# Kernel tuning notes

Measured on AMD Instinct MI355X. Metric: run time of the kernel, lower is better.

Reference implementation:

```python
import jax, jax.numpy as jnp
import numpy as np

B, S = 1024, 64          # batch, num clips (att_size)
R = 1024                 # CG_rnn_size
E = 1024                 # CG_input_encoding_size
CD = 1024                # clip_context_dim
ED = 1024                # event_context_dim
H = 512                  # CG_att_hid_size


def setup_inputs() -> dict:
    key = jax.random.key(0)
    ks = jax.random.split(key, 20)
    s = 0.02
    return {
        "xt": jax.random.normal(ks[0], (B, E), jnp.float32),
        "video": jax.random.normal(ks[1], (B, 1024), jnp.float32),
        "event": jax.random.normal(ks[2], (B, ED), jnp.float32),
        "clip": jax.random.normal(ks[3], (B, S, CD), jnp.float32),
        "clip_mask": jax.random.randint(ks[4], (B, S), 0, 2, jnp.int32),
        "state_h": jax.random.normal(ks[5], (2, B, R), jnp.float32),
        "state_c": jax.random.normal(ks[6], (2, B, R), jnp.float32),
        # LSTMCell 0 (input = event ++ xt -> ED+E)
        "W_ih0": jax.random.normal(ks[7], (4 * R, ED + E), jnp.float32) * s,
        "b_ih0": jnp.zeros((4 * R,), jnp.float32),
        "W_hh0": jax.random.normal(ks[8], (4 * R, R), jnp.float32) * s,
        "b_hh0": jnp.zeros((4 * R,), jnp.float32),
        # LSTMCell 1 (input = att ++ xt -> CD+E)
        "W_ih1": jax.random.normal(ks[9], (4 * R, CD + E), jnp.float32) * s,
        "b_ih1": jnp.zeros((4 * R,), jnp.float32),
        "W_hh1": jax.random.normal(ks[10], (4 * R, R), jnp.float32) * s,
        "b_hh1": jnp.zeros((4 * R,), jnp.float32),
        # Attention params
        "W_ctx": jax.random.normal(ks[11], (H, CD), jnp.float32) * s,
        "b_ctx": jnp.zeros((H,), jnp.float32),
        "W_h2a": jax.random.normal(ks[12], (H, R), jnp.float32) * s,
        "b_h2a": jnp.zeros((H,), jnp.float32),
        "W_alpha": jax.random.normal(ks[13], (1, H), jnp.float32) * s,
        "b_alpha": jnp.zeros((1,), jnp.float32),
    }


def _lstm_cell(x, h, c, W_ih, b_ih, W_hh, b_hh):
    gates = x @ W_ih.T + b_ih + h @ W_hh.T + b_hh  # [B, 4R]
    i, f, g, o = jnp.split(gates, 4, axis=-1)
    i, f, o = jax.nn.sigmoid(i), jax.nn.sigmoid(f), jax.nn.sigmoid(o)
    g = jnp.tanh(g)
    c_new = f * c + i * g
    h_new = o * jnp.tanh(c_new)
    return h_new, c_new


def _attention(h, att_feats, att_mask, W_ctx, b_ctx, W_h2a, b_h2a, W_alpha, b_alpha):
    att = att_feats @ W_ctx.T + b_ctx                 # [B, S, H]
    att_h = h @ W_h2a.T + b_h2a                       # [B, H]
    dot = jnp.tanh(att + att_h[:, None, :])           # [B, S, H]
    scores = (dot @ W_alpha.T + b_alpha)[..., 0]      # [B, S]
    weight = jax.nn.softmax(scores, axis=1)
    m = att_mask.astype(weight.dtype)
    weight = weight * m
    weight = weight / jnp.sum(weight, axis=1, keepdims=True)
    return jnp.einsum('bs,bsd->bd', weight, att_feats)  # [B, CD]


def reference(xt, video, event, clip, clip_mask, state_h, state_c,
              W_ih0, b_ih0, W_hh0, b_hh0, W_ih1, b_ih1, W_hh1, b_hh1,
              W_ctx, b_ctx, W_h2a, b_h2a, W_alpha, b_alpha):
    pre_h1 = state_h[1]
    # stream 0: torch.cat((xt, event), 1)
    h0, c0 = _lstm_cell(jnp.concatenate([xt, event], axis=1),
                        state_h[0], state_c[0], W_ih0, b_ih0, W_hh0, b_hh0)
    att = _attention(pre_h1, clip, clip_mask,
                     W_ctx, b_ctx, W_h2a, b_h2a, W_alpha, b_alpha)
    h1, c1 = _lstm_cell(jnp.concatenate([xt, att], axis=1),
                        state_h[1], state_c[1], W_ih1, b_ih1, W_hh1, b_hh1)
    # dropout layers are identity in eval mode
    output = jnp.concatenate([h0, h1], axis=1)        # [B, 2R]
    new_h = jnp.stack([h0, h1])
    new_c = jnp.stack([c0, c1])
    return output, new_h, new_c
```

## Files before the change

kernel.cpp:

```cpp
#include <hip/hip_runtime.h>

typedef short short8 __attribute__((ext_vector_type(8)));
typedef float floatx4 __attribute__((ext_vector_type(4)));
typedef unsigned short u16;

__device__ __forceinline__ u16 cvt_bf(float x) {
  unsigned u = __float_as_uint(x);
  unsigned r = 0x7FFFu + ((u >> 16) & 1u);
  return (u16)((u + r) >> 16);
}

__device__ __forceinline__ void gll16(const u16* g, u16* l) {
  __builtin_amdgcn_global_load_lds(
      (__attribute__((address_space(1))) void*)(void*)const_cast<u16*>(g),
      (__attribute__((address_space(3))) void*)(void*)l, 16, 0, 0);
}

#define NSEG 11
struct ConvArgs {
  const float* src[NSEG];
  u16* dst[NSEG];
  unsigned lw[NSEG];
  unsigned dstride[NSEG];
  unsigned blk0[NSEG + 1];
};
__global__ __launch_bounds__(256)
void convert_seg(ConvArgs a) {
  const unsigned blk = blockIdx.x;
  int s = 0;
#pragma unroll
  for (int i = 1; i < NSEG; ++i) if (blk >= a.blk0[i]) s = i;
  const unsigned e0 = (blk - a.blk0[s]) * 2048u + threadIdx.x * 8u;
  const float* src = a.src[s] + e0;
  const float4 v0 = *(const float4*)src;
  const float4 v1 = *(const float4*)(src + 4);
  const unsigned row = e0 >> a.lw[s];
  const unsigned col = e0 & ((1u << a.lw[s]) - 1u);
  u16* d = a.dst[s] + (size_t)row * a.dstride[s] + col;
  short8 p;
  p[0] = (short)cvt_bf(v0.x); p[1] = (short)cvt_bf(v0.y);
  p[2] = (short)cvt_bf(v0.z); p[3] = (short)cvt_bf(v0.w);
  p[4] = (short)cvt_bf(v1.x); p[5] = (short)cvt_bf(v1.y);
  p[6] = (short)cvt_bf(v1.z); p[7] = (short)cvt_bf(v1.w);
  *(short8*)d = p;
}

__global__ __launch_bounds__(256, 2)
void gemm_g(const u16* __restrict__ A, int sa,
            const u16* __restrict__ B, int sb,
            const float* __restrict__ bias0, const float* __restrict__ bias1,
            float* __restrict__ out, int N, int K)
{
  __shared__ u16 sA[64 * 64];
  __shared__ u16 sB[128 * 64];

  const int tid = threadIdx.x;
  const int lane = tid & 63, w = tid >> 6;
  const int quad = lane >> 4, l15 = lane & 15;
  const int wm = w >> 1, wn = w & 1;
  const int Mbase = blockIdx.y * 64, Nbase = blockIdx.x * 128;

  const int srow = lane >> 3;
  const int sslot = (lane & 7) ^ (srow & 7);

  floatx4 acc[2][4] = {};

  for (int k0 = 0; k0 < K; k0 += 64) {
    __syncthreads();
#pragma unroll
    for (int j = 0; j < 6; ++j) {
      const int c = w + 4 * j;
      if (c < 8) {
        const int row = c * 8 + srow;
        gll16(A + (size_t)(Mbase + row) * sa + k0 + sslot * 8, &sA[c * 512]);
      } else {
        const int cb = c - 8;
        const int row = cb * 8 + srow;
        gll16(B + (size_t)(Nbase + row) * sb + k0 + sslot * 8, &sB[cb * 512]);
      }
    }
    __syncthreads();

    short8 af[2][2], bf[4][2];
#pragma unroll
    for (int ks = 0; ks < 2; ++ks) {
#pragma unroll
      for (int mt = 0; mt < 2; ++mt) {
        const int row = wm * 32 + mt * 16 + l15;
        const int slot = (ks * 4 + quad) ^ (row & 7);
        af[mt][ks] = *(const short8*)&sA[row * 64 + slot * 8];
      }
#pragma unroll
      for (int nt = 0; nt < 4; ++nt) {
        const int row = wn * 64 + nt * 16 + l15;
        const int slot = (ks * 4 + quad) ^ (row & 7);
        bf[nt][ks] = *(const short8*)&sB[row * 64 + slot * 8];
      }
    }
#pragma unroll
    for (int ks = 0; ks < 2; ++ks)
#pragma unroll
      for (int mt = 0; mt < 2; ++mt)
#pragma unroll
        for (int nt = 0; nt < 4; ++nt)
          acc[mt][nt] = __builtin_amdgcn_mfma_f32_16x16x32_bf16(af[mt][ks], bf[nt][ks], acc[mt][nt], 0, 0, 0);
  }

#pragma unroll
  for (int nt = 0; nt < 4; ++nt) {
    const int col = Nbase + wn * 64 + nt * 16 + l15;
    const float bc = (bias0 ? bias0[col] : 0.f) + (bias1 ? bias1[col] : 0.f);
#pragma unroll
    for (int mt = 0; mt < 2; ++mt) {
      const int rb = Mbase + wm * 32 + mt * 16 + quad * 4;
#pragma unroll
      for (int r = 0; r < 4; ++r)
        out[(size_t)(rb + r) * N + col] = acc[mt][nt][r] + bc;
    }
  }
}

__global__ __launch_bounds__(512)
void clip_scores(const float* __restrict__ clip,
                 const u16* __restrict__ Wc,
                 const float* __restrict__ atth,
                 const float* __restrict__ Walpha,
                 const int* __restrict__ mask,
                 float* __restrict__ wout)
{
  __shared__ u16 sA[64 * 40];
  __shared__ u16 sB[512 * 32];
  __shared__ float wsum[8][64];

  const int b = blockIdx.x;
  const int tid = threadIdx.x;
  const int lane = tid & 63, w = tid >> 6;
  const int quad = lane >> 4, l15 = lane & 15;
  const float* Ab = clip + (size_t)b * 65536;

  floatx4 acc[4][4] = {};

  for (int k0 = 0; k0 < 1024; k0 += 32) {
    __syncthreads();
    {
      const int srow = lane >> 2;
      const int sslot = (lane & 3) ^ (srow & 3);
#pragma unroll
      for (int j = 0; j < 4; ++j) {
        const int c = w + 8 * j;
        const int row = c * 16 + srow;
        gll16(Wc + (size_t)row * 1024 + k0 + sslot * 8, &sB[c * 512]);
      }
    }
    if (w < 4) {
      const int srow = lane >> 2;
      const int scol = (lane & 3) * 8;
      const int row = w * 16 + srow;
      const float* src = Ab + (size_t)row * 1024 + k0 + scol;
      const float4 v0 = *(const float4*)src;
      const float4 v1 = *(const float4*)(src + 4);
      short8 p;
      p[0] = (short)cvt_bf(v0.x); p[1] = (short)cvt_bf(v0.y);
      p[2] = (short)cvt_bf(v0.z); p[3] = (short)cvt_bf(v0.w);
      p[4] = (short)cvt_bf(v1.x); p[5] = (short)cvt_bf(v1.y);
      p[6] = (short)cvt_bf(v1.z); p[7] = (short)cvt_bf(v1.w);
      *(short8*)&sA[row * 40 + scol] = p;
    }
    __syncthreads();

    short8 af[4], bfr[4];
#pragma unroll
    for (int mt = 0; mt < 4; ++mt)
      af[mt] = *(const short8*)&sA[(mt * 16 + l15) * 40 + quad * 8];
#pragma unroll
    for (int nt = 0; nt < 4; ++nt) {
      const int row = w * 64 + nt * 16 + l15;
      const int slot = quad ^ (row & 3);
      bfr[nt] = *(const short8*)&sB[row * 32 + slot * 8];
    }
#pragma unroll
    for (int mt = 0; mt < 4; ++mt)
#pragma unroll
      for (int nt = 0; nt < 4; ++nt)
        acc[mt][nt] = __builtin_amdgcn_mfma_f32_16x16x32_bf16(af[mt], bfr[nt], acc[mt][nt], 0, 0, 0);
  }

  float rs[4][4] = {};
#pragma unroll
  for (int nt = 0; nt < 4; ++nt) {
    const int col = w * 64 + nt * 16 + l15;
    const float wa = Walpha[col];
    const float ah = atth[(size_t)b * 512 + col];
#pragma unroll
    for (int mt = 0; mt < 4; ++mt)
#pragma unroll
      for (int r = 0; r < 4; ++r)
        rs[mt][r] += wa * tanhf(acc[mt][nt][r] + ah);
  }
#pragma unroll
  for (int mt = 0; mt < 4; ++mt)
#pragma unroll
    for (int r = 0; r < 4; ++r) {
      float v = rs[mt][r];
      v += __shfl_xor(v, 1); v += __shfl_xor(v, 2);
      v += __shfl_xor(v, 4); v += __shfl_xor(v, 8);
      if (l15 == 0) wsum[w][mt * 16 + quad * 4 + r] = v;
    }
  __syncthreads();
  if (tid < 64) {
    float s = 0.f;
#pragma unroll
    for (int i = 0; i < 8; ++i) s += wsum[i][tid];
    float mx = s;
#pragma unroll
    for (int d = 32; d; d >>= 1) mx = fmaxf(mx, __shfl_xor(mx, d));
    const float e = expf(s - mx) * (float)mask[b * 64 + tid];
    float den = e;
#pragma unroll
    for (int d = 32; d; d >>= 1) den += __shfl_xor(den, d);
    wout[b * 64 + tid] = e / den;
  }
}

__global__ __launch_bounds__(256)
void ctx_att(const float* __restrict__ clip, const float* __restrict__ wbuf,
             u16* __restrict__ A1)
{
  __shared__ float w[64];
  const int b = blockIdx.x, tid = threadIdx.x;
  if (tid < 64) w[tid] = wbuf[b * 64 + tid];
  __syncthreads();
  const int d4 = tid * 4;
  const float* cb = clip + (size_t)b * 65536 + d4;
  float4 a = make_float4(0.f, 0.f, 0.f, 0.f);
#pragma unroll 8
  for (int s = 0; s < 64; ++s) {
    const float wt = w[s];
    const float4 c = *(const float4*)(cb + (size_t)s * 1024);
    a.x += wt * c.x; a.y += wt * c.y; a.z += wt * c.z; a.w += wt * c.w;
  }
  ushort4 p;
  p.x = cvt_bf(a.x); p.y = cvt_bf(a.y); p.z = cvt_bf(a.z); p.w = cvt_bf(a.w);
  *(ushort4*)&A1[(size_t)b * 3072 + 1024 + d4] = p;
}

__device__ __forceinline__ float sigm(float x) { return 1.0f / (1.0f + expf(-x)); }

__global__ __launch_bounds__(256)
void lstm_ew(const float* __restrict__ gates, const float* __restrict__ cprev,
             float* __restrict__ out, int st)
{
  const int idx = blockIdx.x * 256 + threadIdx.x;
  const int b = idx >> 8;
  const int r4 = (idx & 255) * 4;
  const float* g = gates + (size_t)b * 4096 + r4;
  const float4 gi = *(const float4*)g;
  const float4 gf = *(const float4*)(g + 1024);
  const float4 gg = *(const float4*)(g + 2048);
  const float4 go = *(const float4*)(g + 3072);
  const float4 c  = *(const float4*)(cprev + (size_t)b * 1024 + r4);
  float4 cn, hn;
  cn.x = sigm(gf.x) * c.x + sigm(gi.x) * tanhf(gg.x);  hn.x = sigm(go.x) * tanhf(cn.x);
  cn.y = sigm(gf.y) * c.y + sigm(gi.y) * tanhf(gg.y);  hn.y = sigm(go.y) * tanhf(cn.y);
  cn.z = sigm(gf.z) * c.z + sigm(gi.z) * tanhf(gg.z);  hn.z = sigm(go.z) * tanhf(cn.z);
  cn.w = sigm(gf.w) * c.w + sigm(gi.w) * tanhf(gg.w);  hn.w = sigm(go.w) * tanhf(cn.w);
  *(float4*)(out + (size_t)b * 2048 + st * 1024 + r4) = hn;
  *(float4*)(out + 2097152 + (size_t)st * 1048576 + (size_t)b * 1024 + r4) = hn;
  *(float4*)(out + 4194304 + (size_t)st * 1048576 + (size_t)b * 1024 + r4) = cn;
}

extern "C" void kernel_launch(void* const* d_in, const int* in_sizes, int n_in,
                              void* d_out, int out_size, void* d_ws, size_t ws_size,
                              hipStream_t stream) {
  (void)in_sizes; (void)n_in; (void)out_size; (void)ws_size;
  const float* xt      = (const float*)d_in[0];
  const float* event   = (const float*)d_in[2];
  const float* clip    = (const float*)d_in[3];
  const int*   cmask   = (const int*)d_in[4];
  const float* state_h = (const float*)d_in[5];
  const float* state_c = (const float*)d_in[6];
  const float* W_ih0   = (const float*)d_in[7];
  const float* b_ih0   = (const float*)d_in[8];
  const float* W_hh0   = (const float*)d_in[9];
  const float* b_hh0   = (const float*)d_in[10];
  const float* W_ih1   = (const float*)d_in[11];
  const float* b_ih1   = (const float*)d_in[12];
  const float* W_hh1   = (const float*)d_in[13];
  const float* b_hh1   = (const float*)d_in[14];
  const float* W_ctx   = (const float*)d_in[15];
  const float* b_ctx   = (const float*)d_in[16];
  const float* W_h2a   = (const float*)d_in[17];
  const float* b_h2a   = (const float*)d_in[18];
  const float* W_alpha = (const float*)d_in[19];

  char* w8 = (char*)d_ws;
  float* gates = (float*)(w8 + 0);
  float* att_h = (float*)(w8 + 16777216);
  float* wbuf  = (float*)(w8 + 18874368);
  u16* A0 = (u16*)(w8 + 19136512);
  u16* A1 = (u16*)(w8 + 25427968);
  u16* W0 = (u16*)(w8 + 31719424);
  u16* W1 = (u16*)(w8 + 56885248);
  u16* Wc = (u16*)(w8 + 82051072);
  u16* Wh = (u16*)(w8 + 83099648);

  const float* h0p = state_h;
  const float* h1p = state_h + 1048576;
  const float* c0p = state_c;
  const float* c1p = state_c + 1048576;
  float* out = (float*)d_out;

  ConvArgs ca;
  const float* srcs[NSEG] = {W_ctx, W_h2a, W_ih0, W_hh0, W_ih1, W_hh1,
                             xt, event, h0p, xt, h1p};
  u16* dsts[NSEG] = {Wc, Wh, W0, W0 + 2048, W1, W1 + 2048,
                     A0, A0 + 1024, A0 + 2048, A1, A1 + 2048};
  const unsigned lws[NSEG]  = {10, 10, 11, 10, 11, 10, 10, 10, 10, 10, 10};
  const unsigned dstr[NSEG] = {1024, 1024, 3072, 3072, 3072, 3072,
                               3072, 3072, 3072, 3072, 3072};
  const unsigned nblk[NSEG] = {256, 256, 4096, 2048, 4096, 2048,
                               512, 512, 512, 512, 512};
  unsigned acc_b = 0;
  for (int i = 0; i < NSEG; ++i) {
    ca.src[i] = srcs[i]; ca.dst[i] = dsts[i];
    ca.lw[i] = lws[i]; ca.dstride[i] = dstr[i];
    ca.blk0[i] = acc_b; acc_b += nblk[i];
  }
  ca.blk0[NSEG] = acc_b;
  convert_seg<<<acc_b, 256, 0, stream>>>(ca);

  gemm_g<<<dim3(4, 16), 256, 0, stream>>>(A1 + 2048, 3072, Wh, 1024,
                                          b_h2a, b_ctx, att_h, 512, 1024);

  clip_scores<<<1024, 512, 0, stream>>>(clip, Wc, att_h, W_alpha, cmask, wbuf);

  ctx_att<<<1024, 256, 0, stream>>>(clip, wbuf, A1);

  gemm_g<<<dim3(32, 16), 256, 0, stream>>>(A0, 3072, W0, 3072,
                                           b_ih0, b_hh0, gates, 4096, 3072);
  lstm_ew<<<1024, 256, 0, stream>>>(gates, c0p, out, 0);

  gemm_g<<<dim3(32, 16), 256, 0, stream>>>(A1, 3072, W1, 3072,
                                           b_ih1, b_hh1, gates, 4096, 3072);
  lstm_ew<<<1024, 256, 0, stream>>>(gates, c1p, out, 1);
}
```

Before: 813.2 us.

## Restructure clip scoring as large-tile GEMM, group LSTM GEMMs, use fast activations

Replaces the per-batch clip_scores kernel with a pre-converted bf16 clip tensor and a generic 128x128-tile GEMM. Its epilogue fuses the tanh/W_alpha reduction and accumulates scores through atomics, followed by a separate softmax kernel. The main GEMMs move to 128x128 tiles, and the two LSTM gate GEMMs run as one grouped launch when workspace allows. Workspace is reused, with clip chunked depending on ws_size, and ctx_att reads bf16 clip when available. tanh and sigmoid use fast exp-based approximations, and the atomics make the score sums order-nondeterministic.

Result: faster. 708.4 us (-12.9%).

```diff
diff --git a/kernel.cpp b/kernel.cpp
--- a/kernel.cpp
+++ b/kernel.cpp
@@ -9,27 +9,37 @@
   unsigned r = 0x7FFFu + ((u >> 16) & 1u);
   return (u16)((u + r) >> 16);
 }
-
+__device__ __forceinline__ float bf2f(u16 h) {
+  return __uint_as_float(((unsigned)h) << 16);
+}
 __device__ __forceinline__ void gll16(const u16* g, u16* l) {
   __builtin_amdgcn_global_load_lds(
       (__attribute__((address_space(1))) void*)(void*)const_cast<u16*>(g),
       (__attribute__((address_space(3))) void*)(void*)l, 16, 0, 0);
 }
-
-#define NSEG 11
+__device__ __forceinline__ float fast_tanh(float x) {
+  float t = __expf(-2.f * fabsf(x));
+  float r = 1.f - 2.f * t / (1.f + t);
+  return copysignf(r, x);
+}
+__device__ __forceinline__ float fast_sigm(float x) {
+  return 1.f / (1.f + __expf(-x));
+}
+
+#define MAXSEG 9
 struct ConvArgs {
-  const float* src[NSEG];
-  u16* dst[NSEG];
-  unsigned lw[NSEG];
-  unsigned dstride[NSEG];
-  unsigned blk0[NSEG + 1];
+  const float* src[MAXSEG];
+  u16* dst[MAXSEG];
+  unsigned lw[MAXSEG];
+  unsigned dstride[MAXSEG];
+  unsigned blk0[MAXSEG + 1];
+  int nseg;
 };
 __global__ __launch_bounds__(256)
 void convert_seg(ConvArgs a) {
   const unsigned blk = blockIdx.x;
   int s = 0;
-#pragma unroll
-  for (int i = 1; i < NSEG; ++i) if (blk >= a.blk0[i]) s = i;
+  for (int i = 1; i < a.nseg; ++i) if (blk >= a.blk0[i]) s = i;
   const unsigned e0 = (blk - a.blk0[s]) * 2048u + threadIdx.x * 8u;
   const float* src = a.src[s] + e0;
   const float4 v0 = *(const float4*)src;
@@ -44,207 +54,168 @@
   p[6] = (short)cvt_bf(v1.z); p[7] = (short)cvt_bf(v1.w);
   *(short8*)d = p;
 }
-
-__global__ __launch_bounds__(256, 2)
-void gemm_g(const u16* __restrict__ A, int sa,
-            const u16* __restrict__ B, int sb,
-            const float* __restrict__ bias0, const float* __restrict__ bias1,
-            float* __restrict__ out, int N, int K)
+__global__ __launch_bounds__(256)
+void conv_flat(const float* __restrict__ src, u16* __restrict__ dst) {
+  const size_t e = (size_t)blockIdx.x * 2048 + threadIdx.x * 8;
+  const float4 v0 = *(const float4*)(src + e);
+  const float4 v1 = *(const float4*)(src + e + 4);
+  short8 p;
+  p[0] = (short)cvt_bf(v0.x); p[1] = (short)cvt_bf(v0.y);
+  p[2] = (short)cvt_bf(v0.z); p[3] = (short)cvt_bf(v0.w);
+  p[4] = (short)cvt_bf(v1.x); p[5] = (short)cvt_bf(v1.y);
+  p[6] = (short)cvt_bf(v1.z); p[7] = (short)cvt_bf(v1.w);
+  *(short8*)(dst + e) = p;
+}
+__global__ __launch_bounds__(256)
+void zerof(float* __restrict__ p) { p[blockIdx.x * 256 + threadIdx.x] = 0.f; }
+
+template<int MODE>
+__global__ __launch_bounds__(256, 3)
+void gemm128(const u16* __restrict__ A, int sa, const u16* __restrict__ B, int sb,
+             const float* __restrict__ bias0, const float* __restrict__ bias1,
+             float* __restrict__ out, int N, int K,
+             const float* __restrict__ atth, const float* __restrict__ Walpha,
+             float* __restrict__ scores, int row0,
+             const u16* A2, const u16* B2,
+             const float* bias0b, const float* bias1b, float* out2)
 {
-  __shared__ u16 sA[64 * 64];
+  if (blockIdx.z) { A = A2; B = B2; bias0 = bias0b; bias1 = bias1b; out = out2; }
+  __shared__ u16 sA[128 * 64];
   __shared__ u16 sB[128 * 64];
 
-  const int tid = threadIdx.x;
-  const int lane = tid & 63, w = tid >> 6;
+  const int tid = threadIdx.x, lane = tid & 63, w = tid >> 6;
   const int quad = lane >> 4, l15 = lane & 15;
   const int wm = w >> 1, wn = w & 1;
-  const int Mbase = blockIdx.y * 64, Nbase = blockIdx.x * 128;
-
+  const int Mbase = blockIdx.y * 128, Nbase = blockIdx.x * 128;
   const int srow = lane >> 3;
-  const int sslot = (lane & 7) ^ (srow & 7);
-
-  floatx4 acc[2][4] = {};
+  const int sslot = (lane & 7) ^ srow;
+
+  floatx4 acc[4][4] = {};
 
   for (int k0 = 0; k0 < K; k0 += 64) {
     __syncthreads();
 #pragma unroll
-    for (int j = 0; j < 6; ++j) {
+    for (int j = 0; j < 4; ++j) {
       const int c = w + 4 * j;
-      if (c < 8) {
-        const int row = c * 8 + srow;
-        gll16(A + (size_t)(Mbase + row) * sa + k0 + sslot * 8, &sA[c * 512]);
-      } else {
-        const int cb = c - 8;
-        const int row = cb * 8 + srow;
-        gll16(B + (size_t)(Nbase + row) * sb + k0 + sslot * 8, &sB[cb * 512]);
-      }
+      const int row = c * 8 + srow;
+      gll16(A + (size_t)(Mbase + row) * sa + k0 + sslot * 8, &sA[c * 512]);
+      gll16(B + (size_t)(Nbase + row) * sb + k0 + sslot * 8, &sB[c * 512]);
     }
     __syncthreads();
-
-    short8 af[2][2], bf[4][2];
 #pragma unroll
     for (int ks = 0; ks < 2; ++ks) {
-#pragma unroll
-      for (int mt = 0; mt < 2; ++mt) {
-        const int row = wm * 32 + mt * 16 + l15;
-        const int slot = (ks * 4 + quad) ^ (row & 7);
-        af[mt][ks] = *(const short8*)&sA[row * 64 + slot * 8];
+      short8 af[4], bf[4];
+#pragma unroll
+      for (int mt = 0; mt < 4; ++mt) {
+        const int row = wm * 64 + mt * 16 + l15;
+        af[mt] = *(const short8*)&sA[row * 64 + ((ks * 4 + quad) ^ (row & 7)) * 8];
       }
 #pragma unroll
       for (int nt = 0; nt < 4; ++nt) {
         const int row = wn * 64 + nt * 16 + l15;
-        const int slot = (ks * 4 + quad) ^ (row & 7);
-        bf[nt][ks] = *(const short8*)&sB[row * 64 + slot * 8];
+        bf[nt] = *(const short8*)&sB[row * 64 + ((ks * 4 + quad) ^ (row & 7)) * 8];
       }
-    }
-#pragma unroll
-    for (int ks = 0; ks < 2; ++ks)
-#pragma unroll
-      for (int mt = 0; mt < 2; ++mt)
+#pragma unroll
+      for (int mt = 0; mt < 4; ++mt)
 #pragma unroll
         for (int nt = 0; nt < 4; ++nt)
-          acc[mt][nt] = __builtin_amdgcn_mfma_f32_16x16x32_bf16(af[mt][ks], bf[nt][ks], acc[mt][nt], 0, 0, 0);
-  }
-
-#pragma unroll
-  for (int nt = 0; nt < 4; ++nt) {
-    const int col = Nbase + wn * 64 + nt * 16 + l15;
-    const float bc = (bias0 ? bias0[col] : 0.f) + (bias1 ? bias1[col] : 0.f);
-#pragma unroll
-    for (int mt = 0; mt < 2; ++mt) {
-      const int rb = Mbase + wm * 32 + mt * 16 + quad * 4;
-#pragma unroll
-      for (int r = 0; r < 4; ++r)
-        out[(size_t)(rb + r) * N + col] = acc[mt][nt][r] + bc;
-    }
-  }
-}
-
-__global__ __launch_bounds__(512)
-void clip_scores(const float* __restrict__ clip,
-                 const u16* __restrict__ Wc,
-                 const float* __restrict__ atth,
-                 const float* __restrict__ Walpha,
-                 const int* __restrict__ mask,
-                 float* __restrict__ wout)
+          acc[mt][nt] = __builtin_amdgcn_mfma_f32_16x16x32_bf16(af[mt], bf[nt], acc[mt][nt], 0, 0, 0);
+    }
+  }
+
+  if (MODE == 0) {
+#pragma unroll
+    for (int nt = 0; nt < 4; ++nt) {
+      const int col = Nbase + wn * 64 + nt * 16 + l15;
+      const float bc = bias0[col] + bias1[col];
+#pragma unroll
+      for (int mt = 0; mt < 4; ++mt) {
+        const int rb = Mbase + wm * 64 + mt * 16 + quad * 4;
+#pragma unroll
+        for (int r = 0; r < 4; ++r)
+          out[(size_t)(rb + r) * N + col] = acc[mt][nt][r] + bc;
+      }
+    }
+  } else {
+    const int b = (row0 + Mbase + wm * 64) >> 6;
+    float rs[4][4] = {};
+#pragma unroll
+    for (int nt = 0; nt < 4; ++nt) {
+      const int col = Nbase + wn * 64 + nt * 16 + l15;
+      const float wa = Walpha[col];
+      const float ah = atth[(size_t)b * 512 + col];
+#pragma unroll
+      for (int mt = 0; mt < 4; ++mt)
+#pragma unroll
+        for (int r = 0; r < 4; ++r)
+          rs[mt][r] += wa * fast_tanh(acc[mt][nt][r] + ah);
+    }
+#pragma unroll
+    for (int mt = 0; mt < 4; ++mt)
+#pragma unroll
+      for (int r = 0; r < 4; ++r) {
+        float v = rs[mt][r];
+        v += __shfl_xor(v, 1); v += __shfl_xor(v, 2);
+        v += __shfl_xor(v, 4); v += __shfl_xor(v, 8);
+        if (l15 == 0)
+          atomicAdd(&scores[row0 + Mbase + wm * 64 + mt * 16 + quad * 4 + r], v);
+      }
+  }
+}
+
+__global__ __launch_bounds__(256)
+void softmax_k(const float* __restrict__ scores, const int* __restrict__ mask,
+               float* __restrict__ wbuf)
 {
-  __shared__ u16 sA[64 * 40];
-  __shared__ u16 sB[512 * 32];
-  __shared__ float wsum[8][64];
-
-  const int b = blockIdx.x;
-  const int tid = threadIdx.x;
-  const int lane = tid & 63, w = tid >> 6;
-  const int quad = lane >> 4, l15 = lane & 15;
-  const float* Ab = clip + (size_t)b * 65536;
-
-  floatx4 acc[4][4] = {};
-
-  for (int k0 = 0; k0 < 1024; k0 += 32) {
-    __syncthreads();
-    {
-      const int srow = lane >> 2;
-      const int sslot = (lane & 3) ^ (srow & 3);
-#pragma unroll
-      for (int j = 0; j < 4; ++j) {
-        const int c = w + 8 * j;
-        const int row = c * 16 + srow;
-        gll16(Wc + (size_t)row * 1024 + k0 + sslot * 8, &sB[c * 512]);
-      }
-    }
-    if (w < 4) {
-      const int srow = lane >> 2;
-      const int scol = (lane & 3) * 8;
-      const int row = w * 16 + srow;
-      const float* src = Ab + (size_t)row * 1024 + k0 + scol;
-      const float4 v0 = *(const float4*)src;
-      const float4 v1 = *(const float4*)(src + 4);
-      short8 p;
-      p[0] = (short)cvt_bf(v0.x); p[1] = (short)cvt_bf(v0.y);
-      p[2] = (short)cvt_bf(v0.z); p[3] = (short)cvt_bf(v0.w);
-      p[4] = (short)cvt_bf(v1.x); p[5] = (short)cvt_bf(v1.y);
-      p[6] = (short)cvt_bf(v1.z); p[7] = (short)cvt_bf(v1.w);
-      *(short8*)&sA[row * 40 + scol] = p;
-    }
-    __syncthreads();
-
-    short8 af[4], bfr[4];
-#pragma unroll
-    for (int mt = 0; mt < 4; ++mt)
-      af[mt] = *(const short8*)&sA[(mt * 16 + l15) * 40 + quad * 8];
-#pragma unroll
-    for (int nt = 0; nt < 4; ++nt) {
-      const int row = w * 64 + nt * 16 + l15;
-      const int slot = quad ^ (row & 3);
-      bfr[nt] = *(const short8*)&sB[row * 32 + slot * 8];
-    }
-#pragma unroll
-    for (int mt = 0; mt < 4; ++mt)
-#pragma unroll
-      for (int nt = 0; nt < 4; ++nt)
-        acc[mt][nt] = __builtin_amdgcn_mfma_f32_16x16x32_bf16(af[mt], bfr[nt], acc[mt][nt], 0, 0, 0);
-  }
-
-  float rs[4][4] = {};
-#pragma unroll
-  for (int nt = 0; nt < 4; ++nt) {
-    const int col = w * 64 + nt * 16 + l15;
-    const float wa = Walpha[col];
-    const float ah = atth[(size_t)b * 512 + col];
-#pragma unroll
-    for (int mt = 0; mt < 4; ++mt)
-#pragma unroll
-      for (int r = 0; r < 4; ++r)
-        rs[mt][r] += wa * tanhf(acc[mt][nt][r] + ah);
-  }
-#pragma unroll
-  for (int mt = 0; mt < 4; ++mt)
-#pragma unroll
-    for (int r = 0; r < 4; ++r) {
-      float v = rs[mt][r];
-      v += __shfl_xor(v, 1); v += __shfl_xor(v, 2);
-      v += __shfl_xor(v, 4); v += __shfl_xor(v, 8);
-      if (l15 == 0) wsum[w][mt * 16 + quad * 4 + r] = v;
-    }
-  __syncthreads();
-  if (tid < 64) {
-    float s = 0.f;
-#pragma unroll
-    for (int i = 0; i < 8; ++i) s += wsum[i][tid];
-    float mx = s;
-#pragma unroll
-    for (int d = 32; d; d >>= 1) mx = fmaxf(mx, __shfl_xor(mx, d));
-    const float e = expf(s - mx) * (float)mask[b * 64 + tid];
-    float den = e;
-#pragma unroll
-    for (int d = 32; d; d >>= 1) den += __shfl_xor(den, d);
-    wout[b * 64 + tid] = e / den;
-  }
-}
-
-__global__ __launch_bounds__(256)
-void ctx_att(const float* __restrict__ clip, const float* __restrict__ wbuf,
-             u16* __restrict__ A1)
+  const int b = blockIdx.x * 4 + (threadIdx.x >> 6);
+  const int s = threadIdx.x & 63;
+  const float v = scores[b * 64 + s];
+  float mx = v;
+#pragma unroll
+  for (int d = 32; d; d >>= 1) mx = fmaxf(mx, __shfl_xor(mx, d));
+  const float e = __expf(v - mx) * (float)mask[b * 64 + s];
+  float den = e;
+#pragma unroll
+  for (int d = 32; d; d >>= 1) den += __shfl_xor(den, d);
+  wbuf[b * 64 + s] = e / den;
+}
+
+template<int BF>
+__global__ __launch_bounds__(128)
+void ctx_att(const float* __restrict__ clipf, const u16* __restrict__ clipb,
+             const float* __restrict__ wbuf, u16* __restrict__ A1)
 {
   __shared__ float w[64];
   const int b = blockIdx.x, tid = threadIdx.x;
   if (tid < 64) w[tid] = wbuf[b * 64 + tid];
   __syncthreads();
-  const int d4 = tid * 4;
-  const float* cb = clip + (size_t)b * 65536 + d4;
-  float4 a = make_float4(0.f, 0.f, 0.f, 0.f);
-#pragma unroll 8
-  for (int s = 0; s < 64; ++s) {
-    const float wt = w[s];
-    const float4 c = *(const float4*)(cb + (size_t)s * 1024);
-    a.x += wt * c.x; a.y += wt * c.y; a.z += wt * c.z; a.w += wt * c.w;
-  }
-  ushort4 p;
-  p.x = cvt_bf(a.x); p.y = cvt_bf(a.y); p.z = cvt_bf(a.z); p.w = cvt_bf(a.w);
-  *(ushort4*)&A1[(size_t)b * 3072 + 1024 + d4] = p;
-}
-
-__device__ __forceinline__ float sigm(float x) { return 1.0f / (1.0f + expf(-x)); }
+  const int c8 = tid * 8;
+  float a[8] = {};
+  if (BF) {
+    const u16* base = clipb + (size_t)b * 65536 + c8;
+#pragma unroll 4
+    for (int s = 0; s < 64; ++s) {
+      const float wt = w[s];
+      const short8 c = *(const short8*)(base + (size_t)s * 1024);
+#pragma unroll
+      for (int j = 0; j < 8; ++j) a[j] += wt * bf2f((u16)c[j]);
+    }
+  } else {
+    const float* base = clipf + (size_t)b * 65536 + c8;
+#pragma unroll 4
+    for (int s = 0; s < 64; ++s) {
+      const float wt = w[s];
+      const float4 v0 = *(const float4*)(base + (size_t)s * 1024);
+      const float4 v1 = *(const float4*)(base + (size_t)s * 1024 + 4);
+      a[0] += wt * v0.x; a[1] += wt * v0.y; a[2] += wt * v0.z; a[3] += wt * v0.w;
+      a[4] += wt * v1.x; a[5] += wt * v1.y; a[6] += wt * v1.z; a[7] += wt * v1.w;
+    }
+  }
+  short8 p;
+#pragma unroll
+  for (int j = 0; j < 8; ++j) p[j] = (short)cvt_bf(a[j]);
+  *(short8*)&A1[(size_t)b * 3072 + 1024 + c8] = p;
+}
 
 __global__ __launch_bounds__(256)
 void lstm_ew(const float* __restrict__ gates, const float* __restrict__ cprev,
@@ -260,10 +231,10 @@
   const float4 go = *(const float4*)(g + 3072);
   const float4 c  = *(const float4*)(cprev + (size_t)b * 1024 + r4);
   float4 cn, hn;
-  cn.x = sigm(gf.x) * c.x + sigm(gi.x) * tanhf(gg.x);  hn.x = sigm(go.x) * tanhf(cn.x);
-  cn.y = sigm(gf.y) * c.y + sigm(gi.y) * tanhf(gg.y);  hn.y = sigm(go.y) * tanhf(cn.y);
-  cn.z = sigm(gf.z) * c.z + sigm(gi.z) * tanhf(gg.z);  hn.z = sigm(go.z) * tanhf(cn.z);
-  cn.w = sigm(gf.w) * c.w + sigm(gi.w) * tanhf(gg.w);  hn.w = sigm(go.w) * tanhf(cn.w);
+  cn.x = fast_sigm(gf.x) * c.x + fast_sigm(gi.x) * fast_tanh(gg.x);  hn.x = fast_sigm(go.x) * fast_tanh(cn.x);
+  cn.y = fast_sigm(gf.y) * c.y + fast_sigm(gi.y) * fast_tanh(gg.y);  hn.y = fast_sigm(go.y) * fast_tanh(cn.y);
+  cn.z = fast_sigm(gf.z) * c.z + fast_sigm(gi.z) * fast_tanh(gg.z);  hn.z = fast_sigm(go.z) * fast_tanh(cn.z);
+  cn.w = fast_sigm(gf.w) * c.w + fast_sigm(gi.w) * fast_tanh(gg.w);  hn.w = fast_sigm(go.w) * fast_tanh(cn.w);
   *(float4*)(out + (size_t)b * 2048 + st * 1024 + r4) = hn;
   *(float4*)(out + 2097152 + (size_t)st * 1048576 + (size_t)b * 1024 + r4) = hn;
   *(float4*)(out + 4194304 + (size_t)st * 1048576 + (size_t)b * 1024 + r4) = cn;
@@ -272,7 +243,7 @@
 extern "C" void kernel_launch(void* const* d_in, const int* in_sizes, int n_in,
                               void* d_out, int out_size, void* d_ws, size_t ws_size,
                               hipStream_t stream) {
-  (void)in_sizes; (void)n_in; (void)out_size; (void)ws_size;
+  (void)in_sizes; (void)n_in; (void)out_size;
   const float* xt      = (const float*)d_in[0];
   const float* event   = (const float*)d_in[2];
   const float* clip    = (const float*)d_in[3];
@@ -293,16 +264,25 @@
   const float* b_h2a   = (const float*)d_in[18];
   const float* W_alpha = (const float*)d_in[19];
 
-  char* w8 = (char*)d_ws;
-  float* gates = (float*)(w8 + 0);
-  float* att_h = (float*)(w8 + 16777216);
-  float* wbuf  = (float*)(w8 + 18874368);
-  u16* A0 = (u16*)(w8 + 19136512);
-  u16* A1 = (u16*)(w8 + 25427968);
-  u16* W0 = (u16*)(w8 + 31719424);
-  u16* W1 = (u16*)(w8 + 56885248);
-  u16* Wc = (u16*)(w8 + 82051072);
-  u16* Wh = (u16*)(w8 + 83099648);
+  int NC; bool grouped;
+  if      (ws_size >= 207618048) { NC = 1; grouped = true;  }
+  else if (ws_size >= 106954752) { NC = 4; grouped = true;  }
+  else                           { NC = 8; grouped = false; }
+
+  char* p = (char*)d_ws;
+  float* gates0 = (float*)p; p += 16777216;
+  float* gates1 = gates0;
+  if (grouped) { gates1 = (float*)p; p += 16777216; }
+  u16* A0 = (u16*)p; p += 6291456;
+  u16* A1 = (u16*)p; p += 6291456;
+  u16* W0 = (u16*)p; p += 25165824;
+  u16* Wc = (u16*)p; p += 1048576;
+  u16* Wh = (u16*)p; p += 1048576;
+  u16* clipb = (u16*)p;
+  u16* W1 = (u16*)p;
+  float* atth   = gates0;
+  float* wbuf   = gates0 + 524288;
+  float* scores = gates0 + 589824;
 
   const float* h0p = state_h;
   const float* h1p = state_h + 1048576;
@@ -310,37 +290,74 @@
   const float* c1p = state_c + 1048576;
   float* out = (float*)d_out;
 
-  ConvArgs ca;
-  const float* srcs[NSEG] = {W_ctx, W_h2a, W_ih0, W_hh0, W_ih1, W_hh1,
-                             xt, event, h0p, xt, h1p};
-  u16* dsts[NSEG] = {Wc, Wh, W0, W0 + 2048, W1, W1 + 2048,
-                     A0, A0 + 1024, A0 + 2048, A1, A1 + 2048};
-  const unsigned lws[NSEG]  = {10, 10, 11, 10, 11, 10, 10, 10, 10, 10, 10};
-  const unsigned dstr[NSEG] = {1024, 1024, 3072, 3072, 3072, 3072,
-                               3072, 3072, 3072, 3072, 3072};
-  const unsigned nblk[NSEG] = {256, 256, 4096, 2048, 4096, 2048,
-                               512, 512, 512, 512, 512};
-  unsigned acc_b = 0;
-  for (int i = 0; i < NSEG; ++i) {
-    ca.src[i] = srcs[i]; ca.dst[i] = dsts[i];
-    ca.lw[i] = lws[i]; ca.dstride[i] = dstr[i];
-    ca.blk0[i] = acc_b; acc_b += nblk[i];
-  }
-  ca.blk0[NSEG] = acc_b;
-  convert_seg<<<acc_b, 256, 0, stream>>>(ca);
-
-  gemm_g<<<dim3(4, 16), 256, 0, stream>>>(A1 + 2048, 3072, Wh, 1024,
-                                          b_h2a, b_ctx, att_h, 512, 1024);
-
-  clip_scores<<<1024, 512, 0, stream>>>(clip, Wc, att_h, W_alpha, cmask, wbuf);
-
-  ctx_att<<<1024, 256, 0, stream>>>(clip, wbuf, A1);
-
-  gemm_g<<<dim3(32, 16), 256, 0, stream>>>(A0, 3072, W0, 3072,
-                                           b_ih0, b_hh0, gates, 4096, 3072);
-  lstm_ew<<<1024, 256, 0, stream>>>(gates, c0p, out, 0);
-
-  gemm_g<<<dim3(32, 16), 256, 0, stream>>>(A1, 3072, W1, 3072,
-                                           b_ih1, b_hh1, gates, 4096, 3072);
-  lstm_ew<<<1024, 256, 0, stream>>>(gates, c1p, out, 1);
-}
+  ConvArgs ca{};
+  {
+    const float* srcs[9] = {W_ctx, W_h2a, W_ih0, W_hh0, xt, event, h0p, xt, h1p};
+    u16* dsts[9] = {Wc, Wh, W0, W0 + 2048, A0, A0 + 1024, A0 + 2048, A1, A1 + 2048};
+    const unsigned lws[9]  = {10, 10, 11, 10, 10, 10, 10, 10, 10};
+    const unsigned dstr[9] = {1024, 1024, 3072, 3072, 3072, 3072, 3072, 3072, 3072};
+    const unsigned nblk[9] = {256, 256, 4096, 2048, 512, 512, 512, 512, 512};
+    unsigned acc = 0;
+    for (int i = 0; i < 9; ++i) {
+      ca.src[i] = srcs[i]; ca.dst[i] = dsts[i];
+      ca.lw[i] = lws[i]; ca.dstride[i] = dstr[i];
+      ca.blk0[i] = acc; acc += nblk[i];
+    }
+    ca.blk0[9] = acc; ca.nseg = 9;
+    convert_seg<<<acc, 256, 0, stream>>>(ca);
+  }
+
+  zerof<<<256, 256, 0, stream>>>(scores);
+
+  gemm128<0><<<dim3(4, 8, 1), 256, 0, stream>>>(
+      A1 + 2048, 3072, Wh, 1024, b_h2a, b_ctx, atth, 512, 1024,
+      nullptr, nullptr, nullptr, 0, nullptr, nullptr, nullptr, nullptr, nullptr);
+
+  const int rows = 65536 / NC;
+  for (int c = 0; c < NC; ++c) {
+    conv_flat<<<rows * 1024 / 2048, 256, 0, stream>>>(clip + (size_t)c * rows * 1024, clipb);
+    gemm128<1><<<dim3(4, rows / 128, 1), 256, 0, stream>>>(
+        clipb, 1024, Wc, 1024, nullptr, nullptr, nullptr, 512, 1024,
+        atth, W_alpha, scores, c * rows,
+        nullptr, nullptr, nullptr, nullptr, nullptr);
+  }
+
+  softmax_k<<<256, 256, 0, stream>>>(scores, cmask, wbuf);
+
+  if (NC == 1) ctx_att<1><<<1024, 128, 0, stream>>>(clip, clipb, wbuf, A1);
+  else         ctx_att<0><<<1024, 128, 0, stream>>>(clip, clipb, wbuf, A1);
+
+  ConvArgs cb{};
+  {
+    const float* srcs[2] = {W_ih1, W_hh1};
+    u16* dsts[2] = {W1, W1 + 2048};
+    const unsigned lws[2] = {11, 10};
+    const unsigned nblk[2] = {4096, 2048};
+    unsigned acc = 0;
+    for (int i = 0; i < 2; ++i) {
+      cb.src[i] = srcs[i]; cb.dst[i] = dsts[i];
+      cb.lw[i] = lws[i]; cb.dstride[i] = 3072;
+      cb.blk0[i] = acc; acc += nblk[i];
+    }
+    cb.blk0[2] = acc; cb.nseg = 2;
+    convert_seg<<<acc, 256, 0, stream>>>(cb);
+  }
+
+  if (grouped) {
+    gemm128<0><<<dim3(32, 8, 2), 256, 0, stream>>>(
+        A0, 3072, W0, 3072, b_ih0, b_hh0, gates0, 4096, 3072,
+        nullptr, nullptr, nullptr, 0,
+        A1, W1, b_ih1, b_hh1, gates1);
+    lstm_ew<<<1024, 256, 0, stream>>>(gates0, c0p, out, 0);
+    lstm_ew<<<1024, 256, 0, stream>>>(gates1, c1p, out, 1);
+  } else {
+    gemm128<0><<<dim3(32, 8, 1), 256, 0, stream>>>(
+        A0, 3072, W0, 3072, b_ih0, b_hh0, gates0, 4096, 3072,
+        nullptr, nullptr, nullptr, 0, nullptr, nullptr, nullptr, nullptr, nullptr);
+    lstm_ew<<<1024, 256, 0, stream>>>(gates0, c0p, out, 0);
+    gemm128<0><<<dim3(32, 8, 1), 256, 0, stream>>>(
+        A1, 3072, W1, 3072, b_ih1, b_hh1, gates0, 4096, 3072,
+        nullptr, nullptr, nullptr, 0, nullptr, nullptr, nullptr, nullptr, nullptr);
+    lstm_ew<<<1024, 256, 0, stream>>>(gates0, c1p, out, 1);
+  }
+}
```
